# Kernel tuning notes

Measured on AMD Instinct MI355X. Metric: run time of the kernel, lower is better.

## Reference

```python
import jax, jax.numpy as jnp
import numpy as np

# Config: hidden=2048, num_heads=32, num_kv_heads=8, head_dim=64,
# compression_factor=2 -> r_hidden=1024, kv_dim=num_kv_heads*head_dim=512,
# num_neighbors=16, context_size=1 (no neighbor-repeat path, no cache concat).
H = 2048
NH = 32
NKV = 8
HD = H // NH          # 64
G = NH // NKV         # 4 key-value groups
RH = H // 2           # 1024
KVD = NKV * HD        # 512
B, S, N = 2, 2048, 16


def setup_inputs() -> dict:
    key = jax.random.key(0)
    k1, k2, k3, k4, k5, k6 = jax.random.split(key, 6)
    hidden_states = jax.random.normal(k1, (B, S, H), dtype=jnp.float32)
    retrieved_hidden_states = jax.random.normal(k2, (B, S, N, RH), dtype=jnp.float32)
    # nn.Linear weights are [out_features, in_features], trunc_normal std=in**-0.5
    Wq = jax.random.normal(k3, (NH * HD, H), dtype=jnp.float32) * (H ** -0.5)
    Wk = jax.random.normal(k4, (KVD, RH), dtype=jnp.float32) * (RH ** -0.5)
    Wv = jax.random.normal(k5, (KVD, RH), dtype=jnp.float32) * (RH ** -0.5)
    Wo = jax.random.normal(k6, (H, NH * HD), dtype=jnp.float32) * ((NH * HD) ** -0.5)
    return {
        "hidden_states": hidden_states,
        "retrieved_hidden_states": retrieved_hidden_states,
        "Wq": Wq,
        "Wk": Wk,
        "Wv": Wv,
        "Wo": Wo,
    }


def reference(hidden_states, retrieved_hidden_states, Wq, Wk, Wv, Wo):
    scaler = HD ** -0.5
    # queries: [B,S,H] -> [B,S,NKV,G,HD] (grouped-query layout; avoids
    # materializing the repeat_kv expansion while computing identical math)
    q = (jnp.einsum("bsh,eh->bse", hidden_states, Wq) * scaler)
    q = q.reshape(B, S, NKV, G, HD)
    # keys/values: [B,S,N,RH] -> [B,S,NKV,N,HD]
    k = jnp.einsum("bsnr,er->bsne", retrieved_hidden_states, Wk).reshape(B, S, N, NKV, HD)
    v = jnp.einsum("bsnr,er->bsne", retrieved_hidden_states, Wv).reshape(B, S, N, NKV, HD)
    k = jnp.moveaxis(k, 2, 3)  # [B,S,NKV,N,HD]
    v = jnp.moveaxis(v, 2, 3)
    # per-query attention over its own N retrieved neighbors
    scores = jnp.einsum("bsagd,bsand->bsagn", q, k)  # [B,S,NKV,G,N]
    attn = jax.nn.softmax(scores, axis=-1)
    out = jnp.einsum("bsagn,bsand->bsagd", attn, v)  # [B,S,NKV,G,HD]
    out = out.reshape(B, S, NH * HD)
    return jnp.einsum("bse,he->bsh", out, Wo)
```

## Files before the change

### kernel.cpp

```cpp
#include <hip/hip_runtime.h>
#include <hip/hip_bf16.h>
#include <cstdint>

#define AS1 __attribute__((address_space(1)))
#define AS3 __attribute__((address_space(3)))

typedef __attribute__((ext_vector_type(8))) __bf16 bf16x8;
typedef __attribute__((ext_vector_type(4))) float f32x4;

__device__ inline unsigned short f2bf(float f) {
    unsigned u = __float_as_uint(f);
    u += 0x7fffu + ((u >> 16) & 1);
    return (unsigned short)(u >> 16);
}
__device__ inline float bf_lo(unsigned u) { return __uint_as_float(u << 16); }
__device__ inline float bf_hi(unsigned u) { return __uint_as_float(u & 0xffff0000u); }

__global__ void cast_f32_bf16(const float* __restrict__ src,
                              unsigned short* __restrict__ dst, int n) {
    int i = (blockIdx.x * blockDim.x + threadIdx.x) * 8;
    if (i >= n) return;
    float4 a = *(const float4*)(src + i);
    float4 b = *(const float4*)(src + i + 4);
    ushort4 lo, hi;
    lo.x = f2bf(a.x); lo.y = f2bf(a.y); lo.z = f2bf(a.z); lo.w = f2bf(a.w);
    hi.x = f2bf(b.x); hi.y = f2bf(b.y); hi.z = f2bf(b.z); hi.w = f2bf(b.w);
    *(ushort4*)(dst + i) = lo;
    *(ushort4*)(dst + i + 4) = hi;
}

template <int OUTF>
__global__ __launch_bounds__(256, 2)
void gemm_bt(const unsigned short* __restrict__ A, const unsigned short* __restrict__ B,
             void* __restrict__ Cv, int M, int N, int K, float scale) {
    __shared__ __align__(16) unsigned short As[128 * 32];
    __shared__ __align__(16) unsigned short Bs[128 * 32];

    const int t = threadIdx.x;
    const int w = t >> 6, lane = t & 63;
    const int bx = blockIdx.x, by = blockIdx.y;
    const int wr = w >> 1, wc = w & 1;
    const int quad = lane >> 4, lr = lane & 15;

    f32x4 acc[4][4] = {};

    const unsigned short* gA = A + (size_t)(by * 128 + (t >> 2)) * K + (t & 3) * 8;
    const unsigned short* gB = B + (size_t)(bx * 128 + (t >> 2)) * K + (t & 3) * 8;
    char* aBase = (char*)As + w * 1024;
    char* bBase = (char*)Bs + w * 1024;

    for (int k0 = 0; k0 < K; k0 += 32) {
        __builtin_amdgcn_global_load_lds((const AS1 void*)gA,
                                         (AS3 void*)aBase, 16, 0, 0);
        __builtin_amdgcn_global_load_lds((const AS1 void*)(gA + (size_t)64 * K),
                                         (AS3 void*)(aBase + 4096), 16, 0, 0);
        __builtin_amdgcn_global_load_lds((const AS1 void*)gB,
                                         (AS3 void*)bBase, 16, 0, 0);
        __builtin_amdgcn_global_load_lds((const AS1 void*)(gB + (size_t)64 * K),
                                         (AS3 void*)(bBase + 4096), 16, 0, 0);
        gA += 32; gB += 32;
        __syncthreads();

        bf16x8 af[4], bfr[4];
#pragma unroll
        for (int i = 0; i < 4; i++)
            af[i] = *(const bf16x8*)(As + (wr * 64 + i * 16 + lr) * 32 + quad * 8);
#pragma unroll
        for (int j = 0; j < 4; j++)
            bfr[j] = *(const bf16x8*)(Bs + (wc * 64 + j * 16 + lr) * 32 + quad * 8);
#pragma unroll
        for (int i = 0; i < 4; i++)
#pragma unroll
            for (int j = 0; j < 4; j++)
                acc[i][j] = __builtin_amdgcn_mfma_f32_16x16x32_bf16(
                    af[i], bfr[j], acc[i][j], 0, 0, 0);
        __syncthreads();
    }

#pragma unroll
    for (int i = 0; i < 4; i++) {
        int row0 = by * 128 + wr * 64 + i * 16 + quad * 4;
#pragma unroll
        for (int j = 0; j < 4; j++) {
            int col = bx * 128 + wc * 64 + j * 16 + lr;
#pragma unroll
            for (int r = 0; r < 4; r++) {
                float vv = acc[i][j][r] * scale;
                size_t idx = (size_t)(row0 + r) * N + col;
                if (OUTF) ((float*)Cv)[idx] = vv;
                else      ((unsigned short*)Cv)[idx] = f2bf(vv);
            }
        }
    }
}

__global__ __launch_bounds__(256, 4)
void attn_kernel(const unsigned short* __restrict__ q,
                 const unsigned short* __restrict__ k,
                 const unsigned short* __restrict__ v,
                 unsigned short* __restrict__ ao) {
    __shared__ __align__(16) unsigned short qs[4][4][72];
    __shared__ __align__(16) unsigned short ks[4][16][72];
    __shared__ __align__(16) unsigned short vs[4][16][72];
    __shared__ float ps[4][4][17];

    const int t = threadIdx.x, w = t >> 6, lane = t & 63;
    const int bs = blockIdx.x >> 1;
    const int kv = (blockIdx.x & 1) * 4 + w;

    if (lane < 32) {
        int g = lane >> 3, part = lane & 7;
        *(int4*)(&qs[w][g][part * 8]) =
            *(const int4*)(q + (size_t)bs * 2048 + kv * 256 + lane * 8);
    }
#pragma unroll
    for (int p = 0; p < 2; p++) {
        int n = p * 8 + (lane >> 3), part = lane & 7;
        size_t src = ((size_t)bs * 16 + n) * 512 + kv * 64 + part * 8;
        *(int4*)(&ks[w][n][part * 8]) = *(const int4*)(k + src);
        *(int4*)(&vs[w][n][part * 8]) = *(const int4*)(v + src);
    }
    __syncthreads();

    {
        const int g = lane & 3, n = lane >> 2;
        const unsigned short* qr = qs[w][g];
        const unsigned short* kr = ks[w][n];
        float s = 0.f;
#pragma unroll
        for (int d = 0; d < 64; d += 2) {
            unsigned uq = *(const unsigned*)(qr + d);
            unsigned uk = *(const unsigned*)(kr + d);
            s += bf_lo(uq) * bf_lo(uk) + bf_hi(uq) * bf_hi(uk);
        }
        float m = s;
#pragma unroll
        for (int off = 4; off < 64; off <<= 1) m = fmaxf(m, __shfl_xor(m, off));
        float e = __expf(s - m);
        float sum = e;
#pragma unroll
        for (int off = 4; off < 64; off <<= 1) sum += __shfl_xor(sum, off);
        ps[w][g][n] = e / sum;
    }
    __syncthreads();

    {
        const int g = lane & 3, d0 = (lane >> 2) * 4;
        float o0 = 0, o1 = 0, o2 = 0, o3 = 0;
#pragma unroll
        for (int n = 0; n < 16; n++) {
            float pv = ps[w][g][n];
            unsigned u0 = *(const unsigned*)(&vs[w][n][d0]);
            unsigned u1 = *(const unsigned*)(&vs[w][n][d0 + 2]);
            o0 += pv * bf_lo(u0); o1 += pv * bf_hi(u0);
            o2 += pv * bf_lo(u1); o3 += pv * bf_hi(u1);
        }
        unsigned r0 = ((unsigned)f2bf(o1) << 16) | f2bf(o0);
        unsigned r1 = ((unsigned)f2bf(o3) << 16) | f2bf(o2);
        uint2 rr = make_uint2(r0, r1);
        *(uint2*)(ao + (size_t)bs * 2048 + kv * 256 + g * 64 + d0) = rr;
    }
}

extern "C" void kernel_launch(void* const* d_in, const int* in_sizes, int n_in,
                              void* d_out, int out_size, void* d_ws, size_t ws_size,
                              hipStream_t stream) {
    (void)in_sizes; (void)n_in; (void)out_size; (void)ws_size;
    const float* hs = (const float*)d_in[0];
    const float* rh = (const float*)d_in[1];
    const float* Wq = (const float*)d_in[2];
    const float* Wk = (const float*)d_in[3];
    const float* Wv = (const float*)d_in[4];
    const float* Wo = (const float*)d_in[5];
    float* out = (float*)d_out;

    const int BS = 4096;
    const int H = 2048, RH = 1024, KVD = 512, NN = 16;

    char* ws = (char*)d_ws;
    auto alloc = [&](size_t elems) {
        unsigned short* p = (unsigned short*)ws;
        ws += elems * 2;
        return p;
    };
    unsigned short* hs_b = alloc((size_t)BS * H);
    unsigned short* rh_b = alloc((size_t)BS * NN * RH);
    unsigned short* wq_b = alloc((size_t)H * H);
    unsigned short* wk_b = alloc((size_t)KVD * RH);
    unsigned short* wv_b = alloc((size_t)KVD * RH);
    unsigned short* wo_b = alloc((size_t)H * H);
    unsigned short* q_b  = alloc((size_t)BS * H);
    unsigned short* k_b  = alloc((size_t)BS * NN * KVD);
    unsigned short* v_b  = alloc((size_t)BS * NN * KVD);
    unsigned short* ao_b = hs_b;

    auto cast = [&](const float* s, unsigned short* d, int n) {
        cast_f32_bf16<<<n / 2048, 256, 0, stream>>>(s, d, n);
    };
    cast(hs, hs_b, BS * H);
    cast(rh, rh_b, BS * NN * RH);
    cast(Wq, wq_b, H * H);
    cast(Wk, wk_b, KVD * RH);
    cast(Wv, wv_b, KVD * RH);
    cast(Wo, wo_b, H * H);

    gemm_bt<0><<<dim3(H / 128, BS / 128), 256, 0, stream>>>(
        hs_b, wq_b, q_b, BS, H, H, 0.125f);
    gemm_bt<0><<<dim3(KVD / 128, (BS * NN) / 128), 256, 0, stream>>>(
        rh_b, wk_b, k_b, BS * NN, KVD, RH, 1.0f);
    gemm_bt<0><<<dim3(KVD / 128, (BS * NN) / 128), 256, 0, stream>>>(
        rh_b, wv_b, v_b, BS * NN, KVD, RH, 1.0f);
    attn_kernel<<<BS * 2, 256, 0, stream>>>(q_b, k_b, v_b, ao_b);
    gemm_bt<1><<<dim3(H / 128, BS / 128), 256, 0, stream>>>(
        ao_b, wo_b, out, BS, H, H, 1.0f);
}
```

Before: 771.7 us.

## Fuse K and V projections into one GEMM and merge all casts into one launch

The six f32-to-bf16 cast launches become a single segmented kernel that picks its source and destination by element offset. The separate K and V projection GEMMs become one GEMM with N=1024 over the contiguous Wk|Wv weights. It writes an interleaved K/V buffer that the attention kernel reads with a stride of 1024. This removes a second full read of the large retrieved-states matrix and several launch overheads, at the cost of a wider output buffer and per-thread segment lookup in the cast.

New measurement: 758.8 us. About the same (-1.7%).

```diff
diff --git a/kernel.cpp b/kernel.cpp
--- a/kernel.cpp
+++ b/kernel.cpp
@@ -16,17 +16,29 @@
 __device__ inline float bf_lo(unsigned u) { return __uint_as_float(u << 16); }
 __device__ inline float bf_hi(unsigned u) { return __uint_as_float(u & 0xffff0000u); }
 
-__global__ void cast_f32_bf16(const float* __restrict__ src,
-                              unsigned short* __restrict__ dst, int n) {
-    int i = (blockIdx.x * blockDim.x + threadIdx.x) * 8;
-    if (i >= n) return;
-    float4 a = *(const float4*)(src + i);
-    float4 b = *(const float4*)(src + i + 4);
+struct CastArgs {
+    const float* s[6];
+    unsigned short* d[6];
+    long end[6];
+};
+
+__global__ void cast_all(CastArgs a, long total) {
+    long e = ((long)blockIdx.x * blockDim.x + threadIdx.x) * 8;
+    if (e >= total) return;
+    int seg = 0;
+#pragma unroll
+    for (int i = 0; i < 5; i++) seg += (e >= a.end[seg]) ? 1 : 0;
+    long base = seg ? a.end[seg - 1] : 0;
+    long local = e - base;
+    const float* src = a.s[seg] + local;
+    float4 x = *(const float4*)src;
+    float4 y = *(const float4*)(src + 4);
     ushort4 lo, hi;
-    lo.x = f2bf(a.x); lo.y = f2bf(a.y); lo.z = f2bf(a.z); lo.w = f2bf(a.w);
-    hi.x = f2bf(b.x); hi.y = f2bf(b.y); hi.z = f2bf(b.z); hi.w = f2bf(b.w);
-    *(ushort4*)(dst + i) = lo;
-    *(ushort4*)(dst + i + 4) = hi;
+    lo.x = f2bf(x.x); lo.y = f2bf(x.y); lo.z = f2bf(x.z); lo.w = f2bf(x.w);
+    hi.x = f2bf(y.x); hi.y = f2bf(y.y); hi.z = f2bf(y.z); hi.w = f2bf(y.w);
+    unsigned short* dst = a.d[seg] + local;
+    *(ushort4*)dst = lo;
+    *(ushort4*)(dst + 4) = hi;
 }
 
 template <int OUTF>
@@ -96,8 +108,7 @@
 
 __global__ __launch_bounds__(256, 4)
 void attn_kernel(const unsigned short* __restrict__ q,
-                 const unsigned short* __restrict__ k,
-                 const unsigned short* __restrict__ v,
+                 const unsigned short* __restrict__ kvb,
                  unsigned short* __restrict__ ao) {
     __shared__ __align__(16) unsigned short qs[4][4][72];
     __shared__ __align__(16) unsigned short ks[4][16][72];
@@ -116,9 +127,9 @@
 #pragma unroll
     for (int p = 0; p < 2; p++) {
         int n = p * 8 + (lane >> 3), part = lane & 7;
-        size_t src = ((size_t)bs * 16 + n) * 512 + kv * 64 + part * 8;
-        *(int4*)(&ks[w][n][part * 8]) = *(const int4*)(k + src);
-        *(int4*)(&vs[w][n][part * 8]) = *(const int4*)(v + src);
+        size_t src = ((size_t)bs * 16 + n) * 1024 + kv * 64 + part * 8;
+        *(int4*)(&ks[w][n][part * 8]) = *(const int4*)(kvb + src);
+        *(int4*)(&vs[w][n][part * 8]) = *(const int4*)(kvb + src + 512);
     }
     __syncthreads();
 
@@ -190,27 +201,30 @@
     unsigned short* wv_b = alloc((size_t)KVD * RH);
     unsigned short* wo_b = alloc((size_t)H * H);
     unsigned short* q_b  = alloc((size_t)BS * H);
-    unsigned short* k_b  = alloc((size_t)BS * NN * KVD);
-    unsigned short* v_b  = alloc((size_t)BS * NN * KVD);
+    unsigned short* kv_b = alloc((size_t)BS * NN * 2 * KVD);
     unsigned short* ao_b = hs_b;
-
-    auto cast = [&](const float* s, unsigned short* d, int n) {
-        cast_f32_bf16<<<n / 2048, 256, 0, stream>>>(s, d, n);
-    };
-    cast(hs, hs_b, BS * H);
-    cast(rh, rh_b, BS * NN * RH);
-    cast(Wq, wq_b, H * H);
-    cast(Wk, wk_b, KVD * RH);
-    cast(Wv, wv_b, KVD * RH);
-    cast(Wo, wo_b, H * H);
+    (void)wv_b;
+
+    CastArgs ca;
+    ca.s[0] = hs;  ca.d[0] = hs_b;
+    ca.s[1] = rh;  ca.d[1] = rh_b;
+    ca.s[2] = Wq;  ca.d[2] = wq_b;
+    ca.s[3] = Wk;  ca.d[3] = wk_b;
+    ca.s[4] = Wv;  ca.d[4] = wv_b;
+    ca.s[5] = Wo;  ca.d[5] = wo_b;
+    long sizes[6] = {(long)BS * H, (long)BS * NN * RH, (long)H * H,
+                     (long)KVD * RH, (long)KVD * RH, (long)H * H};
+    long acc = 0;
+    for (int i = 0; i < 6; i++) { acc += sizes[i]; ca.end[i] = acc; }
+    long total = acc;
+    int cast_blocks = (int)((total / 8 + 255) / 256);
+    cast_all<<<cast_blocks, 256, 0, stream>>>(ca, total);
 
     gemm_bt<0><<<dim3(H / 128, BS / 128), 256, 0, stream>>>(
         hs_b, wq_b, q_b, BS, H, H, 0.125f);
-    gemm_bt<0><<<dim3(KVD / 128, (BS * NN) / 128), 256, 0, stream>>>(
-        rh_b, wk_b, k_b, BS * NN, KVD, RH, 1.0f);
-    gemm_bt<0><<<dim3(KVD / 128, (BS * NN) / 128), 256, 0, stream>>>(
-        rh_b, wv_b, v_b, BS * NN, KVD, RH, 1.0f);
-    attn_kernel<<<BS * 2, 256, 0, stream>>>(q_b, k_b, v_b, ao_b);
+    gemm_bt<0><<<dim3((2 * KVD) / 128, (BS * NN) / 128), 256, 0, stream>>>(
+        rh_b, wk_b, kv_b, BS * NN, 2 * KVD, RH, 1.0f);
+    attn_kernel<<<BS * 2, 256, 0, stream>>>(q_b, kv_b, ao_b);
     gemm_bt<1><<<dim3(H / 128, BS / 128), 256, 0, stream>>>(
         ao_b, wo_b, out, BS, H, H, 1.0f);
 }
```
